# Performance work log

Hardware: AMD Instinct MI355X
Metric: run time of the kernel (lower is better)

The kernel has to match this reference:

```python
import jax, jax.numpy as jnp
import numpy as np

B, T, D = 64, 64, 64
E, HA, HB, OUT = 128, 128, 128, 1
SHORT = 2


def _rn(k, shape, scale=0.05):
    return jax.random.normal(k, shape, dtype=jnp.float32) * scale


def setup_inputs() -> dict:
    key = jax.random.key(0)
    ks = jax.random.split(key, 18)
    return {
        "x": jax.random.normal(ks[0], (B, T, D), dtype=jnp.float32),
        "W_emb": _rn(ks[1], (E, D)), "b_emb": _rn(ks[2], (E,)),
        "Wi_a": _rn(ks[3], (3 * HA, E)), "Wh_a": _rn(ks[4], (3 * HA, HA)),
        "bi_a": _rn(ks[5], (3 * HA,)), "bh_a": _rn(ks[6], (3 * HA,)),
        "Wi_b": _rn(ks[7], (3 * HB, E)), "Wh_b": _rn(ks[8], (3 * HB, HB)),
        "bi_b": _rn(ks[9], (3 * HB,)), "bh_b": _rn(ks[10], (3 * HB,)),
        "Wa": _rn(ks[11], (1, HA)), "ba": _rn(ks[12], (1,)),
        "Wb": _rn(ks[13], (E, HB)), "bb": _rn(ks[14], (E,)),
        "Wo": _rn(ks[15], (OUT, E)), "bo": _rn(ks[16], (OUT,)),
        "short": SHORT,
    }


def _gru_cell(x, h, Wi, Wh, bi, bh):
    # PyTorch GRU cell: gates ordered (r, z, n)
    gi = x @ Wi.T + bi
    gh = h @ Wh.T + bh
    ir, iz, in_ = jnp.split(gi, 3, axis=-1)
    hr, hz, hn = jnp.split(gh, 3, axis=-1)
    r = jax.nn.sigmoid(ir + hr)
    z = jax.nn.sigmoid(iz + hz)
    n = jnp.tanh(in_ + r * hn)
    return (1.0 - z) * n + z * h


def _forward(x, W_emb, b_emb, Wi_a, Wh_a, bi_a, bh_a, Wi_b, Wh_b, bi_b, bh_b,
             Wa, ba, Wb, bb, Wo, bo, short):
    Bn, Tn = x.shape[0], x.shape[1]
    temp = jnp.transpose(x, (1, 0, 2))            # [T, B, D]
    emb = temp @ W_emb.T + b_emb                  # [T, B, E]
    P = Tn - 1                                    # prefix p handles att_timesteps t = p+1
    S = Tn - 1                                    # max reversed-prefix length
    p_idx = jnp.arange(P)
    h0a = jnp.zeros((P, Bn, Wh_a.shape[1]), x.dtype)
    h0b = jnp.zeros((P, Bn, Wh_b.shape[1]), x.dtype)

    # All prefixes at once: for prefix p, reversed input at step s is emb[p - s].
    def step(carry, s):
        ha, hb = carry
        j = jnp.clip(p_idx - s, 0, Tn - 1)        # [P]
        e_in = emb[j]                             # [P, B, E]
        x_in = temp[j]                            # [P, B, D]
        na = _gru_cell(e_in, ha, Wi_a, Wh_a, bi_a, bh_a)
        nb = _gru_cell(e_in, hb, Wi_b, Wh_b, bi_b, bh_b)
        valid = (p_idx >= s)[:, None, None]
        ha = jnp.where(valid, na, ha)
        hb = jnp.where(valid, nb, hb)
        return (ha, hb), (ha, hb, e_in, x_in)

    _, (Ha, Hb, Eg, Xg) = jax.lax.scan(step, (h0a, h0b), jnp.arange(S))
    Ha = 0.5 * Ha                                 # reverse_h_a * 0.5, [S, P, B, HA]
    Hb = 0.5 * Hb                                 # reverse_h_b * 0.5, [S, P, B, HB]

    mask = p_idx[None, :] >= jnp.arange(S)[:, None]   # [S, P] valid scan steps
    preA = jnp.einsum('spbh,h->spb', Ha, Wa[0]) + ba[0]
    preA = jnp.where(mask[:, :, None], preA, -jnp.inf)
    alpha = jax.nn.softmax(preA, axis=0)              # softmax over prefix positions
    beta = jnp.tanh(jnp.einsum('spbh,eh->spbe', Hb, Wb) + bb)  # [S, P, B, E]

    # context: c[p] = sum_s alpha * beta * emb[p-s]  (softmax is order-invariant)
    c = jnp.einsum('spb,spbe->pbe', alpha, beta * Eg)          # [P, B, E]
    pred = c @ Wo.T + bo                                        # [P, B, 1]

    # interpretability weights: e = (beta * w_out) @ W_emb, f = alpha*e*x, g = mean over prefix
    e_chain = jnp.einsum('spbe,ed->spbd', beta * Wo[0], W_emb)  # [S, P, B, D]
    f = alpha[..., None] * e_chain * Xg
    g = jnp.sum(f, axis=0) / (p_idx[:, None, None] + 1.0)       # mean over t = p+1 steps

    pred = jnp.transpose(pred[short + 1:], (1, 0, 2))           # [B, T-2-short, 1]
    weight = jnp.transpose(g[short + 1:], (1, 0, 2))            # [B, T-2-short, D]
    return pred, weight


def reference(x, W_emb, b_emb, Wi_a, Wh_a, bi_a, bh_a, Wi_b, Wh_b, bi_b, bh_b,
              Wa, ba, Wb, bb, Wo, bo, short):
    return _forward(x, W_emb, b_emb, Wi_a, Wh_a, bi_a, bh_a, Wi_b, Wh_b, bi_b,
                    bh_b, Wa, ba, Wb, bb, Wo, bo, short)
```

## Files before the change

### kernel.cpp

```cpp
#include <hip/hip_runtime.h>
#include <hip/hip_bf16.h>
#include <math.h>

#define B_ 64
#define T_ 64
#define D_ 64
#define PMIN 3
#define NPOUT 60
#define NCHUNK 4

typedef __hip_bfloat16 bf16;
typedef __attribute__((ext_vector_type(4))) short s16x4;
typedef __attribute__((ext_vector_type(8))) short s16x8;
typedef __attribute__((ext_vector_type(4))) float f32x4;

#define CI_X      0
#define CI_WEMB   262144
#define CI_BEMB   270336
#define CI_WIA    270464
#define CI_WHA    319616
#define CI_BIA    368768
#define CI_BHA    369152
#define CI_WIB    369536
#define CI_WHB    418688
#define CI_BIB    467840
#define CI_BHB    468224
#define CI_WA     468608
#define CI_BA     468736
#define CI_WB     468737
#define CI_BB     485121
#define CI_WO     485249
#define CI_BO     485377
#define CI_TOTAL  485378

#define OFF_EMB   0
#define OFF_WIC   524288
#define OFF_XT    622592
#define OFF_IN    884736
#define OFF_GIPK  1370114
#define OFF_WPK   2942978
#define OFF_BPPK  2992130
#define OFF_WMPK  3000322
#define OFF_WALPK 3004418
#define OFF_FLAG  3005442

__device__ __forceinline__ float bf2f(unsigned short u) {
    union { float f; unsigned u32; } x; x.u32 = ((unsigned)u) << 16; return x.f;
}
__device__ __forceinline__ unsigned short f2bf(float f) {
    union { float f; unsigned u; } x; x.f = f;
    unsigned r = x.u + 0x7FFFu + ((x.u >> 16) & 1u);
    return (unsigned short)(r >> 16);
}
__device__ __forceinline__ float sigmoidf_(float v) { return 1.f / (1.f + __expf(-v)); }
__device__ __forceinline__ float tanhf_(float v) {
    float e = __expf(-2.f * fabsf(v));
    float t = (1.f - e) / (1.f + e);
    return copysignf(t, v);
}
__device__ __forceinline__ int kpi(int s) {
    return (s & ~31) | ((s & 1) << 4) | ((s & 31) >> 1);
}
__device__ __forceinline__ s16x8 ldA(const short* p) {
    s16x4 lo = *(const s16x4*)p;
    s16x4 hi = *(const s16x4*)(p + 4);
    return __builtin_shufflevector(lo, hi, 0, 1, 2, 3, 4, 5, 6, 7);
}

__global__ void detect_dtype(const unsigned short* xr, int* flag)
{
    int tid = threadIdx.x;
    int bad = 0;
    for (int i = tid; i < 4096; i += 256) {
        int ex = (xr[i] >> 7) & 0xFF;
        if (ex >= 140) bad++;
    }
    __shared__ int s[256];
    s[tid] = bad;
    __syncthreads();
    for (int st = 128; st > 0; st >>= 1) {
        if (tid < st) s[tid] += s[tid + st];
        __syncthreads();
    }
    if (tid == 0) *flag = (s[0] > 4) ? 1 : 0;
}

__global__ void convert_inputs(const void* p0, const void* p1, const void* p2,
                               const void* p3, const void* p4, const void* p5,
                               const void* p6, const void* p7, const void* p8,
                               const void* p9, const void* p10, const void* p11,
                               const void* p12, const void* p13, const void* p14,
                               const void* p15, const void* p16,
                               float* ws, const int* flagp)
{
    const int bc[17]     = {1024, 32, 1, 192, 192, 2, 2, 192, 192, 2, 2, 1, 1, 64, 1, 1, 1};
    const int sizes[17]  = {262144, 8192, 128, 49152, 49152, 384, 384, 49152, 49152,
                            384, 384, 128, 1, 16384, 128, 128, 1};
    const int starts[17] = {CI_X, CI_WEMB, CI_BEMB, CI_WIA, CI_WHA, CI_BIA, CI_BHA,
                            CI_WIB, CI_WHB, CI_BIB, CI_BHB, CI_WA, CI_BA, CI_WB,
                            CI_BB, CI_WO, CI_BO};
    int b = blockIdx.x, k = 0;
    while (b >= bc[k]) { b -= bc[k]; k++; }
    int li = b * 256 + threadIdx.x;
    if (li >= sizes[k]) return;
    const void* p;
    switch (k) {
        case 0: p = p0; break;  case 1: p = p1; break;  case 2: p = p2; break;
        case 3: p = p3; break;  case 4: p = p4; break;  case 5: p = p5; break;
        case 6: p = p6; break;  case 7: p = p7; break;  case 8: p = p8; break;
        case 9: p = p9; break;  case 10: p = p10; break; case 11: p = p11; break;
        case 12: p = p12; break; case 13: p = p13; break; case 14: p = p14; break;
        case 15: p = p15; break; default: p = p16; break;
    }
    float v;
    if (*flagp) v = ((const float*)p)[li];
    else        v = bf2f(((const unsigned short*)p)[li]);
    ws[OFF_IN + starts[k] + li] = v;
}

__global__ void prep_all(float* ws)
{
    const float* cin = ws + OFF_IN;
    int id = blockIdx.x * 256 + threadIdx.x;
    if (id < 98304) {
        int e = id / 768, g = id % 768;
        float v = (g < 384) ? cin[CI_WIA + g * 128 + e]
                            : cin[CI_WIB + (g - 384) * 128 + e];
        ws[OFF_WIC + id] = v;
    } else if (id < 622592) {
        int id2 = id - 98304;
        int e = id2 & 127;
        int tb = id2 >> 7;
        int b = tb & 63, t = tb >> 6;
        const float* xp = cin + CI_X + (b * T_ + t) * D_;
        const float* wp = cin + CI_WEMB + e * D_;
        float acc = cin[CI_BEMB + e];
        #pragma unroll
        for (int d = 0; d < 64; d += 4) {
            f32x4 xv = *(const f32x4*)(xp + d);
            f32x4 wv = *(const f32x4*)(wp + d);
            acc += xv[0]*wv[0] + xv[1]*wv[1] + xv[2]*wv[2] + xv[3]*wv[3];
        }
        ws[OFF_EMB + id2] = acc;
    } else if (id < 884736) {
        int id5 = id - 622592;
        int b = id5 & 63, d = (id5 >> 6) & 63, t = id5 >> 12;
        ws[OFF_XT + id5] = cin[CI_X + (b * 64 + t) * 64 + d];
    } else if (id < 983040) {
        unsigned short* wpk = (unsigned short*)(ws + OFF_WPK);
        int id3 = id - 884736;
        int w = id3 / 12288, r1 = id3 % 12288;
        int nt = r1 / 2048, r2 = r1 % 2048;
        int kt = r2 / 512, r3 = r2 % 512;
        int lane = r3 >> 3, j = r3 & 7;
        int cell = w >> 2, wv = w & 3;
        int gate = nt >> 1, tt = nt & 1;
        int g = gate * 128 + wv * 32 + tt * 16 + (lane & 15);
        int k = kpi(kt * 32 + (lane >> 4) * 8 + j);
        wpk[id3] = f2bf(cin[(cell ? CI_WHB : CI_WHA) + g * 128 + k]);
    } else if (id < 999424) {
        unsigned short* bpk = (unsigned short*)(ws + OFF_BPPK);
        int id4 = id - 983040;
        int w = id4 / 2048, r = id4 % 2048;
        int kt = r / 512, lane = (r % 512) >> 3, j = r & 7;
        int e = w * 16 + (lane & 15);
        int k = kpi(kt * 32 + (lane >> 4) * 8 + j);
        bpk[id4] = f2bf(cin[CI_WB + e * 128 + k]);
    } else if (id < 1007616) {
        unsigned short* wmk = (unsigned short*)(ws + OFF_WMPK);
        int id6 = id - 999424;
        int nt = id6 / 2048, r = id6 % 2048;
        int kt = r / 512, lane = (r % 512) >> 3, j = r & 7;
        int d = nt * 16 + (lane & 15);
        int e = kt * 32 + (lane >> 4) * 8 + j;
        wmk[id6] = f2bf(cin[CI_WO + e] * cin[CI_WEMB + e * 64 + d]);
    } else {
        unsigned short* alk = (unsigned short*)(ws + OFF_WALPK);
        int id7 = id - 1007616;
        int kt = id7 / 512, lane = (id7 % 512) >> 3, j = id7 & 7;
        int k = kpi(kt * 32 + (lane >> 4) * 8 + j);
        alk[id7] = ((lane & 15) == 0) ? f2bf(cin[CI_WA + k]) : (unsigned short)0;
    }
}

__global__ void prep_gi(float* ws)
{
    const float* cin = ws + OFF_IN;
    unsigned short* gipk = (unsigned short*)(ws + OFF_GIPK);
    int t = blockIdx.x >> 2;
    int chunk = blockIdx.x & 3;
    int b0 = chunk * 16;
    int tid = threadIdx.x;
    __shared__ __align__(16) float semT[128][16];
    #pragma unroll
    for (int q = 0; q < 8; q++) {
        int idx = tid + q * 256;
        int r = idx & 15, e = idx >> 4;
        semT[e][r] = ws[OFF_EMB + (size_t)((t * 64 + b0 + r) * 128) + e];
    }
    __syncthreads();
    float acc[3][16];
    #pragma unroll
    for (int g3 = 0; g3 < 3; g3++)
        #pragma unroll
        for (int r = 0; r < 16; r++) acc[g3][r] = 0.f;
    const float* wic = ws + OFF_WIC;
    for (int e = 0; e < 128; e++) {
        f32x4 h0 = *(const f32x4*)&semT[e][0];
        f32x4 h1 = *(const f32x4*)&semT[e][4];
        f32x4 h2 = *(const f32x4*)&semT[e][8];
        f32x4 h3 = *(const f32x4*)&semT[e][12];
        float hv[16] = {h0[0],h0[1],h0[2],h0[3], h1[0],h1[1],h1[2],h1[3],
                        h2[0],h2[1],h2[2],h2[3], h3[0],h3[1],h3[2],h3[3]};
        float w0 = wic[e * 768 + tid];
        float w1 = wic[e * 768 + tid + 256];
        float w2 = wic[e * 768 + tid + 512];
        #pragma unroll
        for (int r = 0; r < 16; r++) {
            acc[0][r] += hv[r] * w0;
            acc[1][r] += hv[r] * w1;
            acc[2][r] += hv[r] * w2;
        }
    }
    #pragma unroll
    for (int g3 = 0; g3 < 3; g3++) {
        int g = tid + g3 * 256;
        int cellg = g / 384, gr = g % 384;
        int gate = gr / 128, kh = gr % 128;
        int wvp = kh / 32, tt2 = (kh % 32) / 16, l15p = kh % 16;
        int wq = cellg * 4 + wvp;
        float bias = cin[(cellg ? CI_BIB : CI_BIA) + gr];
        if (gate < 2) bias += cin[(cellg ? CI_BHB : CI_BHA) + gr];
        #pragma unroll
        for (int r = 0; r < 16; r++) {
            float v = acc[g3][r] + bias;
            size_t addr = ((((size_t)t * 4 + chunk) * 8 + wq) * 64
                           + (size_t)((r >> 2) * 16 + l15p)) * 24
                          + gate * 8 + tt2 * 4 + (r & 3);
            gipk[addr] = f2bf(v);
        }
    }
}


__launch_bounds__(512, 2)
__global__ void chain_kernel(const float* ws, void* outv, const int* flagp,
                             const void* p_bha, const void* p_bhb,
                             const void* p_bb, const void* p_ba,
                             const void* p_bo, const void* p_wo)
{
    const int p = PMIN + (int)blockIdx.x / NCHUNK;
    const int chunk = (int)blockIdx.x % NCHUNK;
    const int tid = threadIdx.x;
    const int lane = tid & 63;
    const int w = tid >> 6;
    const int cell = w >> 2;
    const int wv = w & 3;
    const int l15 = lane & 15;
    const int quad = lane >> 4;

    __shared__ __align__(16) short hbf[2][2][16][132];
    __shared__ __align__(16) short betbf[2][16][132];
    __shared__ __align__(16) short sWm[4][4][64][8];
    __shared__ float spaLds[2][16];

    const unsigned short* gipk = (const unsigned short*)(ws + OFF_GIPK);
    const unsigned short* wpk  = (const unsigned short*)(ws + OFF_WPK);
    const unsigned short* bpk  = (const unsigned short*)(ws + OFF_BPPK);
    const unsigned short* alk  = (const unsigned short*)(ws + OFF_WALPK);
    const int flag = *flagp;

    {
        const int* s2 = (const int*)(ws + OFF_WMPK);
        int* d2 = (int*)&sWm[0][0][0][0];
        for (int i = tid; i < 4096; i += 512) d2[i] = s2[i];
        int* hz = (int*)&hbf[0][0][0][0];
        for (int i = tid; i < 2112; i += 512) hz[i] = 0;
    }

    s16x8 wB[6][4];
    #pragma unroll
    for (int nt = 0; nt < 6; nt++)
        #pragma unroll
        for (int kt = 0; kt < 4; kt++)
            wB[nt][kt] = *(const s16x8*)(wpk + (((w * 6 + nt) * 4 + kt) * 64 + lane) * 8);
    s16x8 bBp[4], wAl[4];
    #pragma unroll
    for (int kt = 0; kt < 4; kt++) {
        bBp[kt] = *(const s16x8*)(bpk + ((w * 4 + kt) * 64 + lane) * 8);
        wAl[kt] = *(const s16x8*)(alk + (kt * 64 + lane) * 8);
    }

    float bhn0, bhn1, bbE, baf, bof;
    if (flag) {
        const float* bh = (const float*)(cell ? p_bhb : p_bha);
        bhn0 = bh[256 + wv * 32 + l15];
        bhn1 = bh[256 + wv * 32 + 16 + l15];
        bbE = ((const float*)p_bb)[w * 16 + l15];
        baf = ((const float*)p_ba)[0];
        bof = ((const float*)p_bo)[0];
    } else {
        const unsigned short* bh = (const unsigned short*)(cell ? p_bhb : p_bha);
        bhn0 = bf2f(bh[256 + wv * 32 + l15]);
        bhn1 = bf2f(bh[256 + wv * 32 + 16 + l15]);
        bbE = bf2f(((const unsigned short*)p_bb)[w * 16 + l15]);
        baf = bf2f(((const unsigned short*)p_ba)[0]);
        bof = bf2f(((const unsigned short*)p_bo)[0]);
    }

    float h_old[8];
    #pragma unroll
    for (int i = 0; i < 8; i++) h_old[i] = 0.f;
    float gAccR[4] = {0.f, 0.f, 0.f, 0.f};
    float cAccR[8] = {0.f, 0.f, 0.f, 0.f, 0.f, 0.f, 0.f, 0.f};
    float sl4[4] = {0.f, 0.f, 0.f, 0.f};
    float slB = 0.f;

    s16x8 giv[3], givN[3];
    {
        const unsigned short* gp =
            gipk + ((((size_t)p * 4 + chunk) * 8 + w) * 64 + lane) * 24;
        #pragma unroll
        for (int i = 0; i < 3; i++) giv[i] = *(const s16x8*)(gp + i * 8);
    }

    __syncthreads();

    for (int it = 0; it <= p + 1; it++) {
        const int j = p - it;
        const int jp = j + 1;
        const bool doGru = (j >= 0);
        const bool doAcc = (it > 0);
        const int cur = it & 1;
        const int nxt = cur ^ 1;
        const int dbuf = it & 1;

        if (j > 0) {
            const unsigned short* gp =
                gipk + ((((size_t)(j - 1) * 4 + chunk) * 8 + w) * 64 + lane) * 24;
            #pragma unroll
            for (int i = 0; i < 3; i++) givN[i] = *(const s16x8*)(gp + i * 8);
        }
        f32x4 xv, em0, em1;
        if (doAcc) {
            if (w < 4) {
                xv = *(const f32x4*)(ws + OFF_XT + ((size_t)jp * 64 + w * 16 + l15) * 64
                                     + chunk * 16 + quad * 4);
            } else {
                const int row = quad * 4 + (w - 4);
                const float* ep = ws + OFF_EMB
                                  + ((size_t)jp * 64 + chunk * 16 + row) * 128 + l15 * 8;
                em0 = *(const f32x4*)ep;
                em1 = *(const f32x4*)(ep + 4);
            }
        }

        f32x4 Cg[6], Cbp, Cal;
        #pragma unroll
        for (int nt = 0; nt < 6; nt++) Cg[nt] = (f32x4){0.f,0.f,0.f,0.f};
        Cbp = (f32x4){0.f,0.f,0.f,0.f};
        Cal = (f32x4){0.f,0.f,0.f,0.f};

        #pragma unroll
        for (int kt = 0; kt < 4; kt++) {
            s16x8 aA = ldA(&hbf[cur][0][l15][kt * 32 + quad * 8]);
            s16x8 aB = ldA(&hbf[cur][1][l15][kt * 32 + quad * 8]);
            s16x8 aOwn = cell ? aB : aA;
            #pragma unroll
            for (int nt = 0; nt < 6; nt++)
                Cg[nt] = __builtin_amdgcn_mfma_f32_16x16x32_bf16(aOwn, wB[nt][kt], Cg[nt], 0, 0, 0);
            Cbp = __builtin_amdgcn_mfma_f32_16x16x32_bf16(aB, bBp[kt], Cbp, 0, 0, 0);
            if (w == 7)
                Cal = __builtin_amdgcn_mfma_f32_16x16x32_bf16(aA, wAl[kt], Cal, 0, 0, 0);
        }

        if (w == 7 && l15 == 0) {
            #pragma unroll
            for (int reg = 0; reg < 4; reg++)
                spaLds[dbuf][quad * 4 + reg] = fminf(0.5f * Cal[reg] + baf, 60.f);
        }
        if (doGru) {
            #pragma unroll
            for (int reg = 0; reg < 4; reg++) {
                float hn2[2];
                #pragma unroll
                for (int tt = 0; tt < 2; tt++) {
                    float gir = bf2f((unsigned short)giv[0][tt * 4 + reg]);
                    float giz = bf2f((unsigned short)giv[1][tt * 4 + reg]);
                    float gin = bf2f((unsigned short)giv[2][tt * 4 + reg]);
                    float ghr = Cg[0 + tt][reg];
                    float ghz = Cg[2 + tt][reg];
                    float ghn = Cg[4 + tt][reg] + (tt ? bhn1 : bhn0);
                    float ho  = h_old[tt * 4 + reg];
                    float rr = sigmoidf_(gir + ghr);
                    float zz = sigmoidf_(giz + ghz);
                    float nn = tanhf_(gin + rr * ghn);
                    float hv2 = (1.f - zz) * nn + zz * ho;
                    h_old[tt * 4 + reg] = hv2;
                    hn2[tt] = hv2;
                }
                unsigned pk = (unsigned)f2bf(hn2[0]) | ((unsigned)f2bf(hn2[1]) << 16);
                *(unsigned*)&hbf[nxt][cell][quad * 4 + reg][wv * 32 + l15 * 2] = pk;
            }
        }
        #pragma unroll
        for (int reg = 0; reg < 4; reg++) {
            float bv = tanhf_(0.5f * Cbp[reg] + bbE);
            betbf[dbuf][quad * 4 + reg][w * 16 + l15] = (short)f2bf(bv);
        }

        __syncthreads();

        if (doAcc) {
            if (w < 4) {
                f32x4 ec = (f32x4){0.f,0.f,0.f,0.f};
                #pragma unroll
                for (int kt = 0; kt < 4; kt++) {
                    s16x8 a = ldA(&betbf[dbuf][l15][kt * 32 + quad * 8]);
                    s16x8 bw = *(const s16x8*)&sWm[w][kt][lane][0];
                    ec = __builtin_amdgcn_mfma_f32_16x16x32_bf16(a, bw, ec, 0, 0, 0);
                }
                #pragma unroll
                for (int reg = 0; reg < 4; reg++) {
                    float we = __expf(spaLds[dbuf][quad * 4 + reg]);
                    sl4[reg] += we;
                    gAccR[reg] += we * ec[reg] * xv[reg];
                }
            } else {
                const int row = quad * 4 + (w - 4);
                float we = __expf(spaLds[dbuf][row]);
                slB += we;
                const short* bp2 = &betbf[dbuf][row][l15 * 8];
                s16x4 blo = *(const s16x4*)bp2;
                s16x4 bhi = *(const s16x4*)(bp2 + 4);
                #pragma unroll
                for (int v = 0; v < 4; v++)
                    cAccR[v] += we * bf2f((unsigned short)blo[v]) * em0[v];
                #pragma unroll
                for (int v = 0; v < 4; v++)
                    cAccR[4 + v] += we * bf2f((unsigned short)bhi[v]) * em1[v];
            }
        }

        if (j > 0) { giv[0] = givN[0]; giv[1] = givN[1]; giv[2] = givN[2]; }
    }

    if (w >= 4) {
        const int row = quad * 4 + (w - 4);
        float wo8[8];
        if (flag) {
            const float* wp = (const float*)p_wo + l15 * 8;
            #pragma unroll
            for (int v = 0; v < 8; v++) wo8[v] = wp[v];
        } else {
            const unsigned short* wp = (const unsigned short*)p_wo + l15 * 8;
            #pragma unroll
            for (int v = 0; v < 8; v++) wo8[v] = bf2f(wp[v]);
        }
        float part = 0.f;
        #pragma unroll
        for (int v = 0; v < 8; v++) part += cAccR[v] * wo8[v];
        part += __shfl_xor(part, 1);
        part += __shfl_xor(part, 2);
        part += __shfl_xor(part, 4);
        part += __shfl_xor(part, 8);
        if (l15 == 0) {
            int bglob = chunk * 16 + row;
            float pr = part / slB + bof;
            size_t oi = (size_t)bglob * NPOUT + (p - PMIN);
            if (flag) ((float*)outv)[oi] = pr;
            else      ((bf16*)outv)[oi] = __float2bfloat16(pr);
        }
    } else {
        const float invt = 1.f / (float)(p + 1);
        #pragma unroll
        for (int reg = 0; reg < 4; reg++) {
            int row = quad * 4 + reg;
            int bglob = chunk * 16 + row;
            float gv = gAccR[reg] / sl4[reg] * invt;
            size_t oi = (size_t)B_ * NPOUT
                      + ((size_t)bglob * NPOUT + (p - PMIN)) * 64 + w * 16 + l15;
            if (flag) ((float*)outv)[oi] = gv;
            else      ((bf16*)outv)[oi] = __float2bfloat16(gv);
        }
    }
}

extern "C" void kernel_launch(void* const* d_in, const int* in_sizes, int n_in,
                              void* d_out, int out_size, void* d_ws, size_t ws_size,
                              hipStream_t stream)
{
    float* ws = (float*)d_ws;
    int* flagp = (int*)(ws + OFF_FLAG);

    hipLaunchKernelGGL(detect_dtype, dim3(1), dim3(256), 0, stream,
                       (const unsigned short*)d_in[0], flagp);
    hipLaunchKernelGGL(convert_inputs, dim3(1902), dim3(256), 0, stream,
                       d_in[0], d_in[1], d_in[2], d_in[3], d_in[4], d_in[5],
                       d_in[6], d_in[7], d_in[8], d_in[9], d_in[10], d_in[11],
                       d_in[12], d_in[13], d_in[14], d_in[15], d_in[16],
                       ws, flagp);
    hipLaunchKernelGGL(prep_all, dim3(3944), dim3(256), 0, stream, ws);
    hipLaunchKernelGGL(prep_gi,  dim3(256),  dim3(256), 0, stream, ws);
    hipLaunchKernelGGL(chain_kernel, dim3(NPOUT * NCHUNK), dim3(512), 0, stream,
                       ws, d_out, flagp,
                       d_in[6], d_in[10], d_in[14], d_in[12], d_in[16], d_in[15]);
}
```

Measured before the change: 377.9 us.

## Merge two batch chunks per chain block and stage gate-input writes through LDS

The chain kernel now runs two batch chunks per 1024-thread block, 120 blocks instead of 240. Each half keeps its own hidden-state, beta and attention buffers in LDS, and the shared sWm table is loaded once per block. prep_gi now builds its packed output in shared memory and writes it out with coalesced 16-byte stores instead of scattered 2-byte stores. Workspace offsets shift by two floats so the packed region is 16-byte aligned. The cost is that both halves share one __syncthreads per step, and the register budget per thread is tighter with larger blocks.

```diff
diff --git a/kernel.cpp b/kernel.cpp
--- a/kernel.cpp
+++ b/kernel.cpp
@@ -37,12 +37,12 @@
 #define OFF_WIC   524288
 #define OFF_XT    622592
 #define OFF_IN    884736
-#define OFF_GIPK  1370114
-#define OFF_WPK   2942978
-#define OFF_BPPK  2992130
-#define OFF_WMPK  3000322
-#define OFF_WALPK 3004418
-#define OFF_FLAG  3005442
+#define OFF_GIPK  1370116
+#define OFF_WPK   2942980
+#define OFF_BPPK  2992132
+#define OFF_WMPK  3000324
+#define OFF_WALPK 3004420
+#define OFF_FLAG  3005444
 
 __device__ __forceinline__ float bf2f(unsigned short u) {
     union { float f; unsigned u32; } x; x.u32 = ((unsigned)u) << 16; return x.f;
@@ -192,6 +192,7 @@
     int b0 = chunk * 16;
     int tid = threadIdx.x;
     __shared__ __align__(16) float semT[128][16];
+    __shared__ __align__(16) unsigned short stg[12288];
     #pragma unroll
     for (int q = 0; q < 8; q++) {
         int idx = tid + q * 256;
@@ -234,35 +235,42 @@
         #pragma unroll
         for (int r = 0; r < 16; r++) {
             float v = acc[g3][r] + bias;
-            size_t addr = ((((size_t)t * 4 + chunk) * 8 + wq) * 64
-                           + (size_t)((r >> 2) * 16 + l15p)) * 24
-                          + gate * 8 + tt2 * 4 + (r & 3);
-            gipk[addr] = f2bf(v);
-        }
-    }
-}
-
-
-__launch_bounds__(512, 2)
+            int lane2 = (r >> 2) * 16 + l15p;
+            int slot = gate * 8 + tt2 * 4 + (r & 3);
+            stg[(wq * 64 + lane2) * 24 + slot] = f2bf(v);
+        }
+    }
+    __syncthreads();
+    const uint4* s4 = (const uint4*)stg;
+    uint4* d4 = (uint4*)(gipk + (size_t)(t * 4 + chunk) * 12288);
+    #pragma unroll
+    for (int i = 0; i < 6; i++) d4[tid + i * 256] = s4[tid + i * 256];
+}
+
+
+__launch_bounds__(1024, 4)
 __global__ void chain_kernel(const float* ws, void* outv, const int* flagp,
                              const void* p_bha, const void* p_bhb,
                              const void* p_bb, const void* p_ba,
                              const void* p_bo, const void* p_wo)
 {
-    const int p = PMIN + (int)blockIdx.x / NCHUNK;
-    const int chunk = (int)blockIdx.x % NCHUNK;
+    const int p = PMIN + (int)blockIdx.x / 2;
+    const int pair = (int)blockIdx.x & 1;
     const int tid = threadIdx.x;
     const int lane = tid & 63;
-    const int w = tid >> 6;
+    const int W = tid >> 6;
+    const int half = W >> 3;
+    const int w = W & 7;
+    const int chunk = pair * 2 + half;
     const int cell = w >> 2;
     const int wv = w & 3;
     const int l15 = lane & 15;
     const int quad = lane >> 4;
 
-    __shared__ __align__(16) short hbf[2][2][16][132];
-    __shared__ __align__(16) short betbf[2][16][132];
+    __shared__ __align__(16) short hbf[2][2][2][16][132];
+    __shared__ __align__(16) short betbf[2][2][16][132];
     __shared__ __align__(16) short sWm[4][4][64][8];
-    __shared__ float spaLds[2][16];
+    __shared__ float spaLds[2][2][16];
 
     const unsigned short* gipk = (const unsigned short*)(ws + OFF_GIPK);
     const unsigned short* wpk  = (const unsigned short*)(ws + OFF_WPK);
@@ -273,9 +281,9 @@
     {
         const int* s2 = (const int*)(ws + OFF_WMPK);
         int* d2 = (int*)&sWm[0][0][0][0];
-        for (int i = tid; i < 4096; i += 512) d2[i] = s2[i];
-        int* hz = (int*)&hbf[0][0][0][0];
-        for (int i = tid; i < 2112; i += 512) hz[i] = 0;
+        for (int i = tid; i < 4096; i += 1024) d2[i] = s2[i];
+        int* hz = (int*)&hbf[0][0][0][0][0];
+        for (int i = tid; i < 8448; i += 1024) hz[i] = 0;
     }
 
     s16x8 wB[6][4];
@@ -363,8 +371,8 @@
 
         #pragma unroll
         for (int kt = 0; kt < 4; kt++) {
-            s16x8 aA = ldA(&hbf[cur][0][l15][kt * 32 + quad * 8]);
-            s16x8 aB = ldA(&hbf[cur][1][l15][kt * 32 + quad * 8]);
+            s16x8 aA = ldA(&hbf[half][cur][0][l15][kt * 32 + quad * 8]);
+            s16x8 aB = ldA(&hbf[half][cur][1][l15][kt * 32 + quad * 8]);
             s16x8 aOwn = cell ? aB : aA;
             #pragma unroll
             for (int nt = 0; nt < 6; nt++)
@@ -377,7 +385,7 @@
         if (w == 7 && l15 == 0) {
             #pragma unroll
             for (int reg = 0; reg < 4; reg++)
-                spaLds[dbuf][quad * 4 + reg] = fminf(0.5f * Cal[reg] + baf, 60.f);
+                spaLds[half][dbuf][quad * 4 + reg] = fminf(0.5f * Cal[reg] + baf, 60.f);
         }
         if (doGru) {
             #pragma unroll
@@ -400,13 +408,13 @@
                     hn2[tt] = hv2;
                 }
                 unsigned pk = (unsigned)f2bf(hn2[0]) | ((unsigned)f2bf(hn2[1]) << 16);
-                *(unsigned*)&hbf[nxt][cell][quad * 4 + reg][wv * 32 + l15 * 2] = pk;
+                *(unsigned*)&hbf[half][nxt][cell][quad * 4 + reg][wv * 32 + l15 * 2] = pk;
             }
         }
         #pragma unroll
         for (int reg = 0; reg < 4; reg++) {
             float bv = tanhf_(0.5f * Cbp[reg] + bbE);
-            betbf[dbuf][quad * 4 + reg][w * 16 + l15] = (short)f2bf(bv);
+            betbf[half][dbuf][quad * 4 + reg][w * 16 + l15] = (short)f2bf(bv);
         }
 
         __syncthreads();
@@ -416,21 +424,21 @@
                 f32x4 ec = (f32x4){0.f,0.f,0.f,0.f};
                 #pragma unroll
                 for (int kt = 0; kt < 4; kt++) {
-                    s16x8 a = ldA(&betbf[dbuf][l15][kt * 32 + quad * 8]);
+                    s16x8 a = ldA(&betbf[half][dbuf][l15][kt * 32 + quad * 8]);
                     s16x8 bw = *(const s16x8*)&sWm[w][kt][lane][0];
                     ec = __builtin_amdgcn_mfma_f32_16x16x32_bf16(a, bw, ec, 0, 0, 0);
                 }
                 #pragma unroll
                 for (int reg = 0; reg < 4; reg++) {
-                    float we = __expf(spaLds[dbuf][quad * 4 + reg]);
+                    float we = __expf(spaLds[half][dbuf][quad * 4 + reg]);
                     sl4[reg] += we;
                     gAccR[reg] += we * ec[reg] * xv[reg];
                 }
             } else {
                 const int row = quad * 4 + (w - 4);
-                float we = __expf(spaLds[dbuf][row]);
+                float we = __expf(spaLds[half][dbuf][row]);
                 slB += we;
-                const short* bp2 = &betbf[dbuf][row][l15 * 8];
+                const short* bp2 = &betbf[half][dbuf][row][l15 * 8];
                 s16x4 blo = *(const s16x4*)bp2;
                 s16x4 bhi = *(const s16x4*)(bp2 + 4);
                 #pragma unroll
@@ -502,7 +510,7 @@
                        ws, flagp);
     hipLaunchKernelGGL(prep_all, dim3(3944), dim3(256), 0, stream, ws);
     hipLaunchKernelGGL(prep_gi,  dim3(256),  dim3(256), 0, stream, ws);
-    hipLaunchKernelGGL(chain_kernel, dim3(NPOUT * NCHUNK), dim3(512), 0, stream,
+    hipLaunchKernelGGL(chain_kernel, dim3(NPOUT * 2), dim3(1024), 0, stream,
                        ws, d_out, flagp,
                        d_in[6], d_in[10], d_in[14], d_in[12], d_in[16], d_in[15]);
 }
```

New measurement: 1.275 ms. +237.4%, slower.

## Halve batch chunk per block, drop convert pass, reverse block order

Applied to the files above, without the earlier changes.

The batch chunk per chain block shrinks from 16 to 8 rows, doubling the grid to 480 blocks. The MFMA tiles are still 16 rows, so half of each tile is padding (zeroed in LDS and skipped in stores). The separate convert_inputs kernel is removed and the prep kernels read raw inputs directly, with prep_gi staging its packed output in LDS for coalesced copies. Blocks are launched longest-prefix first to balance the tail, and the gi register prefetch is dropped, which may expose load latency in the recurrence loop.

```diff
diff --git a/kernel.cpp b/kernel.cpp
--- a/kernel.cpp
+++ b/kernel.cpp
@@ -7,42 +7,22 @@
 #define D_ 64
 #define PMIN 3
 #define NPOUT 60
-#define NCHUNK 4
+#define NCHUNK 8
 
 typedef __hip_bfloat16 bf16;
 typedef __attribute__((ext_vector_type(4))) short s16x4;
 typedef __attribute__((ext_vector_type(8))) short s16x8;
 typedef __attribute__((ext_vector_type(4))) float f32x4;
 
-#define CI_X      0
-#define CI_WEMB   262144
-#define CI_BEMB   270336
-#define CI_WIA    270464
-#define CI_WHA    319616
-#define CI_BIA    368768
-#define CI_BHA    369152
-#define CI_WIB    369536
-#define CI_WHB    418688
-#define CI_BIB    467840
-#define CI_BHB    468224
-#define CI_WA     468608
-#define CI_BA     468736
-#define CI_WB     468737
-#define CI_BB     485121
-#define CI_WO     485249
-#define CI_BO     485377
-#define CI_TOTAL  485378
-
 #define OFF_EMB   0
 #define OFF_WIC   524288
 #define OFF_XT    622592
-#define OFF_IN    884736
-#define OFF_GIPK  1370114
-#define OFF_WPK   2942978
-#define OFF_BPPK  2992130
-#define OFF_WMPK  3000322
-#define OFF_WALPK 3004418
-#define OFF_FLAG  3005442
+#define OFF_GIPK  884736
+#define OFF_WPK   2457600
+#define OFF_BPPK  2506752
+#define OFF_WMPK  2514944
+#define OFF_WALPK 2519040
+#define OFF_FLAG  2520064
 
 __device__ __forceinline__ float bf2f(unsigned short u) {
     union { float f; unsigned u32; } x; x.u32 = ((unsigned)u) << 16; return x.f;
@@ -51,6 +31,9 @@
     union { float f; unsigned u; } x; x.f = f;
     unsigned r = x.u + 0x7FFFu + ((x.u >> 16) & 1u);
     return (unsigned short)(r >> 16);
+}
+__device__ __forceinline__ float LDF(const void* p, int i, int flag) {
+    return flag ? ((const float*)p)[i] : bf2f(((const unsigned short*)p)[i]);
 }
 __device__ __forceinline__ float sigmoidf_(float v) { return 1.f / (1.f + __expf(-v)); }
 __device__ __forceinline__ float tanhf_(float v) {
@@ -85,67 +68,44 @@
     if (tid == 0) *flag = (s[0] > 4) ? 1 : 0;
 }
 
-__global__ void convert_inputs(const void* p0, const void* p1, const void* p2,
-                               const void* p3, const void* p4, const void* p5,
-                               const void* p6, const void* p7, const void* p8,
-                               const void* p9, const void* p10, const void* p11,
-                               const void* p12, const void* p13, const void* p14,
-                               const void* p15, const void* p16,
-                               float* ws, const int* flagp)
+__global__ void prep_all(const void* p_x, const void* p_wemb, const void* p_bemb,
+                         const void* p_wia, const void* p_wha,
+                         const void* p_wib, const void* p_whb,
+                         const void* p_wa, const void* p_wb, const void* p_wo,
+                         float* ws, const int* flagp)
 {
-    const int bc[17]     = {1024, 32, 1, 192, 192, 2, 2, 192, 192, 2, 2, 1, 1, 64, 1, 1, 1};
-    const int sizes[17]  = {262144, 8192, 128, 49152, 49152, 384, 384, 49152, 49152,
-                            384, 384, 128, 1, 16384, 128, 128, 1};
-    const int starts[17] = {CI_X, CI_WEMB, CI_BEMB, CI_WIA, CI_WHA, CI_BIA, CI_BHA,
-                            CI_WIB, CI_WHB, CI_BIB, CI_BHB, CI_WA, CI_BA, CI_WB,
-                            CI_BB, CI_WO, CI_BO};
-    int b = blockIdx.x, k = 0;
-    while (b >= bc[k]) { b -= bc[k]; k++; }
-    int li = b * 256 + threadIdx.x;
-    if (li >= sizes[k]) return;
-    const void* p;
-    switch (k) {
-        case 0: p = p0; break;  case 1: p = p1; break;  case 2: p = p2; break;
-        case 3: p = p3; break;  case 4: p = p4; break;  case 5: p = p5; break;
-        case 6: p = p6; break;  case 7: p = p7; break;  case 8: p = p8; break;
-        case 9: p = p9; break;  case 10: p = p10; break; case 11: p = p11; break;
-        case 12: p = p12; break; case 13: p = p13; break; case 14: p = p14; break;
-        case 15: p = p15; break; default: p = p16; break;
-    }
-    float v;
-    if (*flagp) v = ((const float*)p)[li];
-    else        v = bf2f(((const unsigned short*)p)[li]);
-    ws[OFF_IN + starts[k] + li] = v;
-}
-
-__global__ void prep_all(float* ws)
-{
-    const float* cin = ws + OFF_IN;
+    const int flag = *flagp;
     int id = blockIdx.x * 256 + threadIdx.x;
     if (id < 98304) {
         int e = id / 768, g = id % 768;
-        float v = (g < 384) ? cin[CI_WIA + g * 128 + e]
-                            : cin[CI_WIB + (g - 384) * 128 + e];
+        float v = (g < 384) ? LDF(p_wia, g * 128 + e, flag)
+                            : LDF(p_wib, (g - 384) * 128 + e, flag);
         ws[OFF_WIC + id] = v;
     } else if (id < 622592) {
         int id2 = id - 98304;
         int e = id2 & 127;
         int tb = id2 >> 7;
         int b = tb & 63, t = tb >> 6;
-        const float* xp = cin + CI_X + (b * T_ + t) * D_;
-        const float* wp = cin + CI_WEMB + e * D_;
-        float acc = cin[CI_BEMB + e];
-        #pragma unroll
-        for (int d = 0; d < 64; d += 4) {
-            f32x4 xv = *(const f32x4*)(xp + d);
-            f32x4 wv = *(const f32x4*)(wp + d);
-            acc += xv[0]*wv[0] + xv[1]*wv[1] + xv[2]*wv[2] + xv[3]*wv[3];
+        float acc = LDF(p_bemb, e, flag);
+        if (flag) {
+            const float* xp = (const float*)p_x + (b * T_ + t) * D_;
+            const float* wp = (const float*)p_wemb + e * D_;
+            #pragma unroll
+            for (int d = 0; d < 64; d += 4) {
+                f32x4 xv = *(const f32x4*)(xp + d);
+                f32x4 wv = *(const f32x4*)(wp + d);
+                acc += xv[0]*wv[0] + xv[1]*wv[1] + xv[2]*wv[2] + xv[3]*wv[3];
+            }
+        } else {
+            const unsigned short* xp = (const unsigned short*)p_x + (b * T_ + t) * D_;
+            const unsigned short* wp = (const unsigned short*)p_wemb + e * D_;
+            for (int d = 0; d < 64; d++) acc += bf2f(xp[d]) * bf2f(wp[d]);
         }
         ws[OFF_EMB + id2] = acc;
     } else if (id < 884736) {
         int id5 = id - 622592;
         int b = id5 & 63, d = (id5 >> 6) & 63, t = id5 >> 12;
-        ws[OFF_XT + id5] = cin[CI_X + (b * 64 + t) * 64 + d];
+        ws[OFF_XT + id5] = LDF(p_x, (b * 64 + t) * 64 + d, flag);
     } else if (id < 983040) {
         unsigned short* wpk = (unsigned short*)(ws + OFF_WPK);
         int id3 = id - 884736;
@@ -157,7 +117,7 @@
         int gate = nt >> 1, tt = nt & 1;
         int g = gate * 128 + wv * 32 + tt * 16 + (lane & 15);
         int k = kpi(kt * 32 + (lane >> 4) * 8 + j);
-        wpk[id3] = f2bf(cin[(cell ? CI_WHB : CI_WHA) + g * 128 + k]);
+        wpk[id3] = f2bf(LDF(cell ? p_whb : p_wha, g * 128 + k, flag));
     } else if (id < 999424) {
         unsigned short* bpk = (unsigned short*)(ws + OFF_BPPK);
         int id4 = id - 983040;
@@ -165,7 +125,7 @@
         int kt = r / 512, lane = (r % 512) >> 3, j = r & 7;
         int e = w * 16 + (lane & 15);
         int k = kpi(kt * 32 + (lane >> 4) * 8 + j);
-        bpk[id4] = f2bf(cin[CI_WB + e * 128 + k]);
+        bpk[id4] = f2bf(LDF(p_wb, e * 128 + k, flag));
     } else if (id < 1007616) {
         unsigned short* wmk = (unsigned short*)(ws + OFF_WMPK);
         int id6 = id - 999424;
@@ -173,50 +133,50 @@
         int kt = r / 512, lane = (r % 512) >> 3, j = r & 7;
         int d = nt * 16 + (lane & 15);
         int e = kt * 32 + (lane >> 4) * 8 + j;
-        wmk[id6] = f2bf(cin[CI_WO + e] * cin[CI_WEMB + e * 64 + d]);
+        wmk[id6] = f2bf(LDF(p_wo, e, flag) * LDF(p_wemb, e * 64 + d, flag));
     } else {
         unsigned short* alk = (unsigned short*)(ws + OFF_WALPK);
         int id7 = id - 1007616;
         int kt = id7 / 512, lane = (id7 % 512) >> 3, j = id7 & 7;
         int k = kpi(kt * 32 + (lane >> 4) * 8 + j);
-        alk[id7] = ((lane & 15) == 0) ? f2bf(cin[CI_WA + k]) : (unsigned short)0;
-    }
-}
-
-__global__ void prep_gi(float* ws)
+        alk[id7] = ((lane & 15) == 0) ? f2bf(LDF(p_wa, k, flag)) : (unsigned short)0;
+    }
+}
+
+__global__ void prep_gi(float* ws, const void* p_bia, const void* p_bha,
+                        const void* p_bib, const void* p_bhb, const int* flagp)
 {
-    const float* cin = ws + OFF_IN;
+    const int flag = *flagp;
     unsigned short* gipk = (unsigned short*)(ws + OFF_GIPK);
-    int t = blockIdx.x >> 2;
-    int chunk = blockIdx.x & 3;
-    int b0 = chunk * 16;
+    int t = blockIdx.x >> 3;
+    int chunk = blockIdx.x & 7;
+    int b0 = chunk * 8;
     int tid = threadIdx.x;
-    __shared__ __align__(16) float semT[128][16];
-    #pragma unroll
-    for (int q = 0; q < 8; q++) {
+    __shared__ __align__(16) float semT[128][8];
+    __shared__ __align__(16) unsigned short stg[6144];
+    #pragma unroll
+    for (int q = 0; q < 4; q++) {
         int idx = tid + q * 256;
-        int r = idx & 15, e = idx >> 4;
+        int r = idx & 7, e = idx >> 3;
         semT[e][r] = ws[OFF_EMB + (size_t)((t * 64 + b0 + r) * 128) + e];
     }
     __syncthreads();
-    float acc[3][16];
+    float acc[3][8];
     #pragma unroll
     for (int g3 = 0; g3 < 3; g3++)
         #pragma unroll
-        for (int r = 0; r < 16; r++) acc[g3][r] = 0.f;
+        for (int r = 0; r < 8; r++) acc[g3][r] = 0.f;
     const float* wic = ws + OFF_WIC;
+    #pragma unroll 2
     for (int e = 0; e < 128; e++) {
         f32x4 h0 = *(const f32x4*)&semT[e][0];
         f32x4 h1 = *(const f32x4*)&semT[e][4];
-        f32x4 h2 = *(const f32x4*)&semT[e][8];
-        f32x4 h3 = *(const f32x4*)&semT[e][12];
-        float hv[16] = {h0[0],h0[1],h0[2],h0[3], h1[0],h1[1],h1[2],h1[3],
-                        h2[0],h2[1],h2[2],h2[3], h3[0],h3[1],h3[2],h3[3]};
+        float hv[8] = {h0[0],h0[1],h0[2],h0[3], h1[0],h1[1],h1[2],h1[3]};
         float w0 = wic[e * 768 + tid];
         float w1 = wic[e * 768 + tid + 256];
         float w2 = wic[e * 768 + tid + 512];
         #pragma unroll
-        for (int r = 0; r < 16; r++) {
+        for (int r = 0; r < 8; r++) {
             acc[0][r] += hv[r] * w0;
             acc[1][r] += hv[r] * w1;
             acc[2][r] += hv[r] * w2;
@@ -229,17 +189,20 @@
         int gate = gr / 128, kh = gr % 128;
         int wvp = kh / 32, tt2 = (kh % 32) / 16, l15p = kh % 16;
         int wq = cellg * 4 + wvp;
-        float bias = cin[(cellg ? CI_BIB : CI_BIA) + gr];
-        if (gate < 2) bias += cin[(cellg ? CI_BHB : CI_BHA) + gr];
-        #pragma unroll
-        for (int r = 0; r < 16; r++) {
+        float bias = LDF(cellg ? p_bib : p_bia, gr, flag);
+        if (gate < 2) bias += LDF(cellg ? p_bhb : p_bha, gr, flag);
+        #pragma unroll
+        for (int r = 0; r < 8; r++) {
             float v = acc[g3][r] + bias;
-            size_t addr = ((((size_t)t * 4 + chunk) * 8 + wq) * 64
-                           + (size_t)((r >> 2) * 16 + l15p)) * 24
-                          + gate * 8 + tt2 * 4 + (r & 3);
-            gipk[addr] = f2bf(v);
-        }
-    }
+            int lane2 = (r >> 2) * 16 + l15p;
+            int slot = gate * 8 + tt2 * 4 + (r & 3);
+            stg[(wq * 32 + lane2) * 24 + slot] = f2bf(v);
+        }
+    }
+    __syncthreads();
+    const uint4* s4 = (const uint4*)stg;
+    uint4* d4 = (uint4*)(gipk + (size_t)(t * 8 + chunk) * 6144);
+    for (int i = tid; i < 768; i += 256) d4[i] = s4[i];
 }
 
 
@@ -249,7 +212,7 @@
                              const void* p_bb, const void* p_ba,
                              const void* p_bo, const void* p_wo)
 {
-    const int p = PMIN + (int)blockIdx.x / NCHUNK;
+    const int p = PMIN + (NPOUT - 1) - (int)blockIdx.x / NCHUNK;
     const int chunk = (int)blockIdx.x % NCHUNK;
     const int tid = threadIdx.x;
     const int lane = tid & 63;
@@ -262,7 +225,7 @@
     __shared__ __align__(16) short hbf[2][2][16][132];
     __shared__ __align__(16) short betbf[2][16][132];
     __shared__ __align__(16) short sWm[4][4][64][8];
-    __shared__ float spaLds[2][16];
+    __shared__ float spaLds[2][8];
 
     const unsigned short* gipk = (const unsigned short*)(ws + OFF_GIPK);
     const unsigned short* wpk  = (const unsigned short*)(ws + OFF_WPK);
@@ -275,7 +238,9 @@
         int* d2 = (int*)&sWm[0][0][0][0];
         for (int i = tid; i < 4096; i += 512) d2[i] = s2[i];
         int* hz = (int*)&hbf[0][0][0][0];
-        for (int i = tid; i < 2112; i += 512) hz[i] = 0;
+        for (int i = tid; i < 4224; i += 512) hz[i] = 0;
+        int* bz = (int*)&betbf[0][0][0];
+        for (int i = tid; i < 2112; i += 512) bz[i] = 0;
     }
 
     s16x8 wB[6][4];
@@ -311,18 +276,9 @@
     float h_old[8];
     #pragma unroll
     for (int i = 0; i < 8; i++) h_old[i] = 0.f;
-    float gAccR[4] = {0.f, 0.f, 0.f, 0.f};
-    float cAccR[8] = {0.f, 0.f, 0.f, 0.f, 0.f, 0.f, 0.f, 0.f};
-    float sl4[4] = {0.f, 0.f, 0.f, 0.f};
-    float slB = 0.f;
-
-    s16x8 giv[3], givN[3];
-    {
-        const unsigned short* gp =
-            gipk + ((((size_t)p * 4 + chunk) * 8 + w) * 64 + lane) * 24;
-        #pragma unroll
-        for (int i = 0; i < 3; i++) giv[i] = *(const s16x8*)(gp + i * 8);
-    }
+    float accR[9];
+    #pragma unroll
+    for (int i = 0; i < 9; i++) accR[i] = 0.f;
 
     __syncthreads();
 
@@ -335,21 +291,22 @@
         const int nxt = cur ^ 1;
         const int dbuf = it & 1;
 
-        if (j > 0) {
+        s16x8 giv[3];
+        if (doGru) {
             const unsigned short* gp =
-                gipk + ((((size_t)(j - 1) * 4 + chunk) * 8 + w) * 64 + lane) * 24;
-            #pragma unroll
-            for (int i = 0; i < 3; i++) givN[i] = *(const s16x8*)(gp + i * 8);
+                gipk + ((((size_t)j * 8 + chunk) * 8 + w) * 32 + (lane & 31)) * 24;
+            #pragma unroll
+            for (int i = 0; i < 3; i++) giv[i] = *(const s16x8*)(gp + i * 8);
         }
         f32x4 xv, em0, em1;
         if (doAcc) {
             if (w < 4) {
                 xv = *(const f32x4*)(ws + OFF_XT + ((size_t)jp * 64 + w * 16 + l15) * 64
-                                     + chunk * 16 + quad * 4);
+                                     + chunk * 8 + (quad & 1) * 4);
             } else {
-                const int row = quad * 4 + (w - 4);
+                const int row8 = (quad * 4 + (w - 4)) & 7;
                 const float* ep = ws + OFF_EMB
-                                  + ((size_t)jp * 64 + chunk * 16 + row) * 128 + l15 * 8;
+                                  + ((size_t)jp * 64 + chunk * 8 + row8) * 128 + l15 * 8;
                 em0 = *(const f32x4*)ep;
                 em1 = *(const f32x4*)(ep + 4);
             }
@@ -363,8 +320,10 @@
 
         #pragma unroll
         for (int kt = 0; kt < 4; kt++) {
-            s16x8 aA = ldA(&hbf[cur][0][l15][kt * 32 + quad * 8]);
             s16x8 aB = ldA(&hbf[cur][1][l15][kt * 32 + quad * 8]);
+            s16x8 aA;
+            if (cell == 0 || w == 7) aA = ldA(&hbf[cur][0][l15][kt * 32 + quad * 8]);
+            else aA = aB;
             s16x8 aOwn = cell ? aB : aA;
             #pragma unroll
             for (int nt = 0; nt < 6; nt++)
@@ -374,12 +333,12 @@
                 Cal = __builtin_amdgcn_mfma_f32_16x16x32_bf16(aA, wAl[kt], Cal, 0, 0, 0);
         }
 
-        if (w == 7 && l15 == 0) {
+        if (w == 7 && l15 == 0 && quad < 2) {
             #pragma unroll
             for (int reg = 0; reg < 4; reg++)
                 spaLds[dbuf][quad * 4 + reg] = fminf(0.5f * Cal[reg] + baf, 60.f);
         }
-        if (doGru) {
+        if (doGru && quad < 2) {
             #pragma unroll
             for (int reg = 0; reg < 4; reg++) {
                 float hn2[2];
@@ -403,10 +362,12 @@
                 *(unsigned*)&hbf[nxt][cell][quad * 4 + reg][wv * 32 + l15 * 2] = pk;
             }
         }
-        #pragma unroll
-        for (int reg = 0; reg < 4; reg++) {
-            float bv = tanhf_(0.5f * Cbp[reg] + bbE);
-            betbf[dbuf][quad * 4 + reg][w * 16 + l15] = (short)f2bf(bv);
+        if (quad < 2) {
+            #pragma unroll
+            for (int reg = 0; reg < 4; reg++) {
+                float bv = tanhf_(0.5f * Cbp[reg] + bbE);
+                betbf[dbuf][quad * 4 + reg][w * 16 + l15] = (short)f2bf(bv);
+            }
         }
 
         __syncthreads();
@@ -422,27 +383,25 @@
                 }
                 #pragma unroll
                 for (int reg = 0; reg < 4; reg++) {
-                    float we = __expf(spaLds[dbuf][quad * 4 + reg]);
-                    sl4[reg] += we;
-                    gAccR[reg] += we * ec[reg] * xv[reg];
+                    float we = __expf(spaLds[dbuf][(quad * 4 + reg) & 7]);
+                    accR[4 + reg] += we;
+                    accR[reg] += we * ec[reg] * xv[reg];
                 }
             } else {
-                const int row = quad * 4 + (w - 4);
-                float we = __expf(spaLds[dbuf][row]);
-                slB += we;
-                const short* bp2 = &betbf[dbuf][row][l15 * 8];
+                const int row8 = (quad * 4 + (w - 4)) & 7;
+                float we = __expf(spaLds[dbuf][row8]);
+                accR[8] += we;
+                const short* bp2 = &betbf[dbuf][row8][l15 * 8];
                 s16x4 blo = *(const s16x4*)bp2;
                 s16x4 bhi = *(const s16x4*)(bp2 + 4);
                 #pragma unroll
                 for (int v = 0; v < 4; v++)
-                    cAccR[v] += we * bf2f((unsigned short)blo[v]) * em0[v];
+                    accR[v] += we * bf2f((unsigned short)blo[v]) * em0[v];
                 #pragma unroll
                 for (int v = 0; v < 4; v++)
-                    cAccR[4 + v] += we * bf2f((unsigned short)bhi[v]) * em1[v];
+                    accR[4 + v] += we * bf2f((unsigned short)bhi[v]) * em1[v];
             }
         }
-
-        if (j > 0) { giv[0] = givN[0]; giv[1] = givN[1]; giv[2] = givN[2]; }
     }
 
     if (w >= 4) {
@@ -459,25 +418,25 @@
         }
         float part = 0.f;
         #pragma unroll
-        for (int v = 0; v < 8; v++) part += cAccR[v] * wo8[v];
+        for (int v = 0; v < 8; v++) part += accR[v] * wo8[v];
         part += __shfl_xor(part, 1);
         part += __shfl_xor(part, 2);
         part += __shfl_xor(part, 4);
         part += __shfl_xor(part, 8);
-        if (l15 == 0) {
-            int bglob = chunk * 16 + row;
-            float pr = part / slB + bof;
+        if (l15 == 0 && row < 8) {
+            int bglob = chunk * 8 + row;
+            float pr = part / accR[8] + bof;
             size_t oi = (size_t)bglob * NPOUT + (p - PMIN);
             if (flag) ((float*)outv)[oi] = pr;
             else      ((bf16*)outv)[oi] = __float2bfloat16(pr);
         }
-    } else {
+    } else if (quad < 2) {
         const float invt = 1.f / (float)(p + 1);
         #pragma unroll
         for (int reg = 0; reg < 4; reg++) {
             int row = quad * 4 + reg;
-            int bglob = chunk * 16 + row;
-            float gv = gAccR[reg] / sl4[reg] * invt;
+            int bglob = chunk * 8 + row;
+            float gv = accR[reg] / accR[4 + reg] * invt;
             size_t oi = (size_t)B_ * NPOUT
                       + ((size_t)bglob * NPOUT + (p - PMIN)) * 64 + w * 16 + l15;
             if (flag) ((float*)outv)[oi] = gv;
@@ -495,13 +454,12 @@
 
     hipLaunchKernelGGL(detect_dtype, dim3(1), dim3(256), 0, stream,
                        (const unsigned short*)d_in[0], flagp);
-    hipLaunchKernelGGL(convert_inputs, dim3(1902), dim3(256), 0, stream,
-                       d_in[0], d_in[1], d_in[2], d_in[3], d_in[4], d_in[5],
-                       d_in[6], d_in[7], d_in[8], d_in[9], d_in[10], d_in[11],
-                       d_in[12], d_in[13], d_in[14], d_in[15], d_in[16],
+    hipLaunchKernelGGL(prep_all, dim3(3944), dim3(256), 0, stream,
+                       d_in[0], d_in[1], d_in[2], d_in[3], d_in[4],
+                       d_in[7], d_in[8], d_in[11], d_in[13], d_in[15],
                        ws, flagp);
-    hipLaunchKernelGGL(prep_all, dim3(3944), dim3(256), 0, stream, ws);
-    hipLaunchKernelGGL(prep_gi,  dim3(256),  dim3(256), 0, stream, ws);
+    hipLaunchKernelGGL(prep_gi, dim3(512), dim3(256), 0, stream,
+                       ws, d_in[5], d_in[6], d_in[9], d_in[10], flagp);
     hipLaunchKernelGGL(chain_kernel, dim3(NPOUT * NCHUNK), dim3(512), 0, stream,
                        ws, d_out, flagp,
                        d_in[6], d_in[10], d_in[14], d_in[12], d_in[16], d_in[15]);
```

Result: faster. 354.5 us (-6.2%).
